# Kernel tuning notes

Hardware: AMD Instinct MI355X
Metric: run time of the kernel (lower is better)

The kernel has to match this reference:

```python
import jax, jax.numpy as jnp
import numpy as np

NUM_USERS = 100000
NUM_ITEMS = 50000
N_NODES = NUM_USERS + NUM_ITEMS
D = 64                 # embed_dim (= user/item/cate embed dims)
NNZ = 2400000          # sparse adjacency nnz (avg degree 16)
B = 4096               # batch size
HIST = 50              # item history length (max)
UHIST = 30             # user history length (max)
MC = 5                 # max categories per item
NC = 1000              # num_cates
CONCAT = 3 * D         # 192 = user/item concat dim
INNER = 2 * CONCAT     # 384 = MLP expansion factor 2
NUM_GNN_LAYERS = 3


def setup_inputs() -> dict:
    ks = jax.random.split(jax.random.key(0), 20)
    emb_table = jax.random.normal(ks[0], (N_NODES, D), jnp.float32) * 0.02
    cate_table = jax.random.normal(ks[1], (NC, D), jnp.float32) * 0.02
    adj_rows = jax.random.randint(ks[2], (NNZ,), 0, N_NODES, jnp.int32)
    adj_cols = jax.random.randint(ks[3], (NNZ,), 0, N_NODES, jnp.int32)
    adj_vals = jax.random.uniform(ks[4], (NNZ,), jnp.float32) * (1.0 / 16.0)
    cates = jax.random.randint(ks[5], (NUM_ITEMS, MC), 0, NC, jnp.int32)
    cate_lens = jax.random.randint(ks[6], (NUM_ITEMS,), 1, MC + 1, jnp.int32)
    users = jax.random.randint(ks[7], (B,), 0, NUM_USERS, jnp.int32)
    items = jax.random.randint(ks[8], (B,), 0, NUM_ITEMS, jnp.int32)
    item_history_matrix = jax.random.randint(ks[9], (B, HIST), 0, NUM_ITEMS, jnp.int32)
    item_history_len = jax.random.randint(ks[10], (B,), 1, HIST + 1, jnp.int32)
    user_history_matrix = jax.random.randint(ks[11], (B, UHIST), 0, NUM_USERS, jnp.int32)
    user_history_len = jax.random.randint(ks[12], (B,), 1, UHIST + 1, jnp.int32)
    # 4 PreNormResidual MLP blocks: [user_mlp, user_mlp_2, item_mlp, item_mlp_2]
    mlp_ln_w = jnp.ones((4, CONCAT), jnp.float32)
    mlp_ln_b = jnp.zeros((4, CONCAT), jnp.float32)
    mlp_w1 = jax.random.normal(ks[13], (4, CONCAT, INNER), jnp.float32) * 0.05
    mlp_b1 = jnp.zeros((4, INNER), jnp.float32)
    mlp_w2 = jax.random.normal(ks[14], (4, INNER, CONCAT), jnp.float32) * 0.05
    mlp_b2 = jnp.zeros((4, CONCAT), jnp.float32)
    return dict(emb_table=emb_table, cate_table=cate_table, adj_vals=adj_vals,
                mlp_ln_w=mlp_ln_w, mlp_ln_b=mlp_ln_b, mlp_w1=mlp_w1, mlp_b1=mlp_b1,
                mlp_w2=mlp_w2, mlp_b2=mlp_b2, adj_rows=adj_rows, adj_cols=adj_cols,
                cates=cates, cate_lens=cate_lens, users=users, items=items,
                item_history_matrix=item_history_matrix, item_history_len=item_history_len,
                user_history_matrix=user_history_matrix, user_history_len=user_history_len)


def _avg_pool(emb, lens):
    # emb: [..., L, D], lens: [...] -> masked mean over L (matches average_pooling)
    L = emb.shape[-2]
    mask = (jnp.arange(L) < lens[..., None]).astype(emb.dtype)[..., None]
    s = jnp.sum(emb * mask, axis=-2)
    c = jnp.sum(mask, axis=-2) + 1e-9
    return s / c


def _layernorm(x, w, b, eps=1e-5):
    mu = jnp.mean(x, axis=-1, keepdims=True)
    var = jnp.mean(jnp.square(x - mu), axis=-1, keepdims=True)
    return (x - mu) * jax.lax.rsqrt(var + eps) * w + b


def _forward(emb_table, cate_table, adj_vals, mlp_ln_w, mlp_ln_b, mlp_w1, mlp_b1,
             mlp_w2, mlp_b2, adj_rows, adj_cols, cates, cate_lens, users, items,
             item_history_matrix, item_history_len, user_history_matrix, user_history_len):
    n = emb_table.shape[0]
    # GNN propagation: mean of [e0, e1, e2, e3], e_{k+1} = A @ e_k (SpMM via segment_sum)
    e = emb_table
    acc = emb_table
    for _ in range(NUM_GNN_LAYERS):
        msgs = adj_vals[:, None] * e[adj_cols]          # [nnz, D]
        e = jax.ops.segment_sum(msgs, adj_rows, num_segments=n)
        acc = acc + e
    gnn = acc / float(NUM_GNN_LAYERS + 1)
    # --- user features ---
    static_u = gnn[users]                               # [B, D]
    hist_item = emb_table[item_history_matrix + NUM_USERS]   # [B, H, D]
    hc = cates[item_history_matrix]                     # [B, H, MC]
    hcl = cate_lens[item_history_matrix]                # [B, H]
    hce = cate_table[hc]                                # [B, H, MC, D]
    avg_cate = _avg_pool(hce, hcl)                      # [B, H, D]
    hist_with_cate = jnp.concatenate([hist_item, avg_cate], axis=-1)  # [B, H, 2D]
    user_hist = _avg_pool(hist_with_cate, item_history_len)           # [B, 2D]
    uf = jnp.concatenate([static_u, user_hist], axis=-1)              # [B, 3D]
    # --- item features ---
    static_i = gnn[items + NUM_USERS]                   # [B, D]
    ice = cate_table[cates[items]]                      # [B, MC, D]
    avg_ic = _avg_pool(ice, cate_lens[items])           # [B, D]
    item_with_cate = jnp.concatenate([static_i, avg_ic], axis=-1)     # [B, 2D]
    hu = emb_table[user_history_matrix]                 # [B, Hu, D]
    item_hist = _avg_pool(hu, user_history_len)         # [B, D]
    itf = jnp.concatenate([item_with_cate, item_hist], axis=-1)       # [B, 3D]
    # --- PreNormResidual MLP blocks ---
    def block(x, i):
        y = _layernorm(x, mlp_ln_w[i], mlp_ln_b[i])
        h = jax.nn.relu(y @ mlp_w1[i] + mlp_b1[i])
        return h @ mlp_w2[i] + mlp_b2[i] + x
    ue = block(uf, 0) + block(uf, 1)
    ie = block(itf, 2) + block(itf, 3)
    ue = ue / jnp.maximum(jnp.linalg.norm(ue, axis=-1, keepdims=True), 1e-12)
    ie = ie / jnp.maximum(jnp.linalg.norm(ie, axis=-1, keepdims=True), 1e-12)
    return ue, ie


def reference(emb_table, cate_table, adj_vals, mlp_ln_w, mlp_ln_b, mlp_w1, mlp_b1,
              mlp_w2, mlp_b2, adj_rows, adj_cols, cates, cate_lens, users, items,
              item_history_matrix, item_history_len, user_history_matrix, user_history_len):
    return _forward(emb_table, cate_table, adj_vals, mlp_ln_w, mlp_ln_b, mlp_w1, mlp_b1,
                    mlp_w2, mlp_b2, adj_rows, adj_cols, cates, cate_lens, users, items,
                    item_history_matrix, item_history_len, user_history_matrix, user_history_len)
```

## Files before the change

### kernel.cpp

```cpp
#include <hip/hip_runtime.h>
#include <hip/hip_bf16.h>
#include <cstdint>
#include <cstddef>

#define NU      100000
#define NN      150000
#define DDIM    64
#define NNZ_C   2400000
#define B_C     4096
#define HIST_C  50
#define UHIST_C 30
#define MC_C    5
#define CDIM    192
#define IDIM    384
#define SCAN_B  147
#define SCAN_N  (SCAN_B * 1024)
#define MAXF    96256
#define CAP     44
#define EDGE_BLKS 1172
#define FEAT_BLKS 2048
#define CONV_BLKS 2304
#define EMBC_BLKS 1172

typedef __bf16 bf16x8 __attribute__((ext_vector_type(8)));
typedef __bf16 bf16x4 __attribute__((ext_vector_type(4)));
typedef float f32x4 __attribute__((ext_vector_type(4)));

__device__ inline float4 ldb(const __bf16* p) {
  bf16x4 v = *(const bf16x4*)p;
  return make_float4((float)v[0], (float)v[1], (float)v[2], (float)v[3]);
}
__device__ inline void stb(__bf16* p, float4 o) {
  bf16x4 v;
  v[0] = (__bf16)o.x; v[1] = (__bf16)o.y; v[2] = (__bf16)o.z; v[3] = (__bf16)o.w;
  *(bf16x4*)p = v;
}

__device__ inline void xr4(float4& a) {
  a.x += __shfl_xor(a.x, 16, 64); a.y += __shfl_xor(a.y, 16, 64);
  a.z += __shfl_xor(a.z, 16, 64); a.w += __shfl_xor(a.w, 16, 64);
  a.x += __shfl_xor(a.x, 32, 64); a.y += __shfl_xor(a.y, 32, 64);
  a.z += __shfl_xor(a.z, 32, 64); a.w += __shfl_xor(a.w, 32, 64);
}

__global__ __launch_bounds__(256) void seedflag_kernel(
    const int* __restrict__ users, const int* __restrict__ items,
    int* __restrict__ sf, int* __restrict__ flag) {
  int t = blockIdx.x * 256 + threadIdx.x;
  if (t >= 2 * B_C) return;
  int s = (t < B_C) ? users[t] : items[t - B_C] + NU;
  sf[s] = 1;
  flag[s] = 1;
}

__global__ __launch_bounds__(256) void mega_kernel(
    const int* __restrict__ rows, const int* __restrict__ cols,
    const float* __restrict__ vals, const int* __restrict__ sf,
    int* __restrict__ flag, int* __restrict__ deg, int2* __restrict__ edgp,
    const float* __restrict__ emb, const float* __restrict__ cate_table,
    const int* __restrict__ cates, const int* __restrict__ cate_lens,
    const int* __restrict__ items, const int* __restrict__ ihm,
    const int* __restrict__ ihl, const int* __restrict__ uhm,
    const int* __restrict__ uhl, float* __restrict__ uf,
    float* __restrict__ itf,
    const float* __restrict__ w1, const float* __restrict__ w2,
    __bf16* __restrict__ w1t, __bf16* __restrict__ w2t,
    __bf16* __restrict__ embbf) {
  int blk = blockIdx.x;
  if (blk < EDGE_BLKS) {
    int base = blk * 2048 + threadIdx.x;
#pragma unroll
    for (int k = 0; k < 8; ++k) {
      int e = base + k * 256;
      if (e < NNZ_C) {
        int r = rows[e];
        int p = atomicAdd(&deg[r], 1);
        if (p < CAP)
          edgp[(size_t)r * CAP + p] = make_int2(cols[e], __float_as_int(vals[e]));
        if (sf[r]) flag[cols[e]] = 1;
      }
    }
  } else if (blk < EDGE_BLKS + FEAT_BLKS) {
    int tid = threadIdx.x;
    int wave = tid >> 6, w = tid & 63, g = w >> 4, li = w & 15;
    int q = (blk - EDGE_BLKS) * 4 + wave;
    if (q < B_C) {
      int b = q;
      int len = ihl[b];
      float4 su = {0.f, 0.f, 0.f, 0.f}, sc = {0.f, 0.f, 0.f, 0.f};
      for (int h = g; h < len; h += 4) {
        int it = ihm[b * HIST_C + h];
        const float4 iv = *(const float4*)(emb + ((size_t)NU + it) * DDIM + li * 4);
        su.x += iv.x; su.y += iv.y; su.z += iv.z; su.w += iv.w;
        int cl = cate_lens[it];
        float4 cs = {0.f, 0.f, 0.f, 0.f};
        for (int c = 0; c < cl; ++c) {
          const float4 cv = *(const float4*)(cate_table + (size_t)cates[it * MC_C + c] * DDIM + li * 4);
          cs.x += cv.x; cs.y += cv.y; cs.z += cv.z; cs.w += cv.w;
        }
        float icl = 1.f / (float)cl;
        sc.x += cs.x * icl; sc.y += cs.y * icl; sc.z += cs.z * icl; sc.w += cs.w * icl;
      }
      xr4(su); xr4(sc);
      float inv = 1.f / (float)len;
      float* urow = uf + (size_t)b * CDIM;
      if (g == 0) {
        float4 o = {su.x * inv, su.y * inv, su.z * inv, su.w * inv};
        *(float4*)(urow + 64 + li * 4) = o;
      } else if (g == 1) {
        float4 o = {sc.x * inv, sc.y * inv, sc.z * inv, sc.w * inv};
        *(float4*)(urow + 128 + li * 4) = o;
      }
    } else {
      int b = q - B_C;
      int it = items[b];
      int cl = cate_lens[it];
      float4 cs = {0.f, 0.f, 0.f, 0.f};
      for (int c = g; c < cl; c += 4) {
        const float4 cv = *(const float4*)(cate_table + (size_t)cates[it * MC_C + c] * DDIM + li * 4);
        cs.x += cv.x; cs.y += cv.y; cs.z += cv.z; cs.w += cv.w;
      }
      int ul = uhl[b];
      float4 hs = {0.f, 0.f, 0.f, 0.f};
      for (int h = g; h < ul; h += 4) {
        const float4 hv = *(const float4*)(emb + (size_t)uhm[b * UHIST_C + h] * DDIM + li * 4);
        hs.x += hv.x; hs.y += hv.y; hs.z += hv.z; hs.w += hv.w;
      }
      xr4(cs); xr4(hs);
      float* irow = itf + (size_t)b * CDIM;
      if (g == 0) {
        float icl = 1.f / (float)cl;
        float4 o = {cs.x * icl, cs.y * icl, cs.z * icl, cs.w * icl};
        *(float4*)(irow + 64 + li * 4) = o;
      } else if (g == 1) {
        float iul = 1.f / (float)ul;
        float4 o = {hs.x * iul, hs.y * iul, hs.z * iul, hs.w * iul};
        *(float4*)(irow + 128 + li * 4) = o;
      }
    }
  } else if (blk < EDGE_BLKS + FEAT_BLKS + CONV_BLKS) {
    int id = (blk - EDGE_BLKS - FEAT_BLKS) * 256 + threadIdx.x;
    if (id < 4 * CDIM * IDIM) {
      int k = id % CDIM;
      int rest = id / CDIM;
      int n = rest % IDIM;
      int p = rest / IDIM;
      w1t[id] = (__bf16)w1[((size_t)(p * CDIM) + k) * IDIM + n];
    } else {
      int id2 = id - 4 * CDIM * IDIM;
      int k = id2 % IDIM;
      int rest = id2 / IDIM;
      int n = rest % CDIM;
      int p = rest / CDIM;
      w2t[id2] = (__bf16)w2[((size_t)(p * IDIM) + k) * CDIM + n];
    }
  } else {
    int base = (blk - EDGE_BLKS - FEAT_BLKS - CONV_BLKS) * 2048 + threadIdx.x;
#pragma unroll
    for (int k = 0; k < 8; ++k) {
      int gidx = base + k * 256;
      if (gidx < 2400000) {
        float4 v = ((const float4*)emb)[gidx];
        stb(embbf + (size_t)gidx * 4, v);
      }
    }
  }
}

__global__ __launch_bounds__(1024) void scan_reduce(
    const int* __restrict__ arr, int* __restrict__ bsums) {
  __shared__ int s[1024];
  int t = threadIdx.x;
  s[t] = arr[blockIdx.x * 1024 + t];
  __syncthreads();
  for (int off = 512; off; off >>= 1) {
    if (t < off) s[t] += s[t + off];
    __syncthreads();
  }
  if (t == 0) bsums[blockIdx.x] = s[0];
}

__global__ __launch_bounds__(1024) void compact_scan(
    int* __restrict__ flag, const int* __restrict__ bsums2,
    int* __restrict__ list, int* __restrict__ cnt) {
  __shared__ int pre[1024];
  __shared__ int s[1024];
  int t = threadIdx.x;
  pre[t] = (t < (int)blockIdx.x) ? bsums2[t] : 0;
  __syncthreads();
  for (int off = 512; off; off >>= 1) {
    if (t < off) pre[t] += pre[t + off];
    __syncthreads();
  }
  int base = pre[0];
  __syncthreads();
  int i = blockIdx.x * 1024 + t;
  int v = flag[i];
  s[t] = v;
  __syncthreads();
  for (int off = 1; off < 1024; off <<= 1) {
    int u = (t >= off) ? s[t - off] : 0;
    __syncthreads();
    s[t] += u;
    __syncthreads();
  }
  int slot = base + s[t] - v;
  if (v) {
    if (slot < MAXF) { list[slot] = i; flag[i] = slot + 1; }
    else flag[i] = 0;
  }
  if (i == SCAN_N - 1) {
    int tot = base + s[t];
    cnt[0] = (tot < MAXF) ? tot : MAXF;
  }
}

__global__ __launch_bounds__(256) void spmm_gather4(
    const __bf16* __restrict__ srcbf, __bf16* __restrict__ dstbf,
    const int* __restrict__ deg, const int2* __restrict__ edgp) {
  int tid = threadIdx.x;
  int wave = tid >> 6, w = tid & 63, g = w >> 4, li = w & 15;
  int r = blockIdx.x * 16 + wave * 4 + g;
  int n = deg[r]; if (n > CAP) n = CAP;
  const int2* ep = edgp + (size_t)r * CAP;
  float4 a0 = {0.f, 0.f, 0.f, 0.f}, a1 = {0.f, 0.f, 0.f, 0.f};
  float4 a2 = {0.f, 0.f, 0.f, 0.f}, a3 = {0.f, 0.f, 0.f, 0.f};
  int j = 0;
  for (; j + 8 <= n; j += 8) {
    int2 e0 = ep[j], e1 = ep[j + 1], e2 = ep[j + 2], e3 = ep[j + 3];
    int2 e4 = ep[j + 4], e5 = ep[j + 5], e6 = ep[j + 6], e7 = ep[j + 7];
    const float4 s0 = ldb(srcbf + (size_t)e0.x * DDIM + li * 4);
    const float4 s1 = ldb(srcbf + (size_t)e1.x * DDIM + li * 4);
    const float4 s2 = ldb(srcbf + (size_t)e2.x * DDIM + li * 4);
    const float4 s3 = ldb(srcbf + (size_t)e3.x * DDIM + li * 4);
    const float4 s4 = ldb(srcbf + (size_t)e4.x * DDIM + li * 4);
    const float4 s5 = ldb(srcbf + (size_t)e5.x * DDIM + li * 4);
    const float4 s6 = ldb(srcbf + (size_t)e6.x * DDIM + li * 4);
    const float4 s7 = ldb(srcbf + (size_t)e7.x * DDIM + li * 4);
    float v0 = __int_as_float(e0.y), v1 = __int_as_float(e1.y);
    float v2 = __int_as_float(e2.y), v3 = __int_as_float(e3.y);
    float v4 = __int_as_float(e4.y), v5 = __int_as_float(e5.y);
    float v6 = __int_as_float(e6.y), v7 = __int_as_float(e7.y);
    a0.x += v0 * s0.x; a0.y += v0 * s0.y; a0.z += v0 * s0.z; a0.w += v0 * s0.w;
    a1.x += v1 * s1.x; a1.y += v1 * s1.y; a1.z += v1 * s1.z; a1.w += v1 * s1.w;
    a2.x += v2 * s2.x; a2.y += v2 * s2.y; a2.z += v2 * s2.z; a2.w += v2 * s2.w;
    a3.x += v3 * s3.x; a3.y += v3 * s3.y; a3.z += v3 * s3.z; a3.w += v3 * s3.w;
    a0.x += v4 * s4.x; a0.y += v4 * s4.y; a0.z += v4 * s4.z; a0.w += v4 * s4.w;
    a1.x += v5 * s5.x; a1.y += v5 * s5.y; a1.z += v5 * s5.z; a1.w += v5 * s5.w;
    a2.x += v6 * s6.x; a2.y += v6 * s6.y; a2.z += v6 * s6.z; a2.w += v6 * s6.w;
    a3.x += v7 * s7.x; a3.y += v7 * s7.y; a3.z += v7 * s7.z; a3.w += v7 * s7.w;
  }
  for (; j + 2 <= n; j += 2) {
    int2 e0 = ep[j], e1 = ep[j + 1];
    const float4 s0 = ldb(srcbf + (size_t)e0.x * DDIM + li * 4);
    const float4 s1 = ldb(srcbf + (size_t)e1.x * DDIM + li * 4);
    float v0 = __int_as_float(e0.y), v1 = __int_as_float(e1.y);
    a0.x += v0 * s0.x; a0.y += v0 * s0.y; a0.z += v0 * s0.z; a0.w += v0 * s0.w;
    a1.x += v1 * s1.x; a1.y += v1 * s1.y; a1.z += v1 * s1.z; a1.w += v1 * s1.w;
  }
  if (j < n) {
    int2 e0 = ep[j];
    const float4 s0 = ldb(srcbf + (size_t)e0.x * DDIM + li * 4);
    float v0 = __int_as_float(e0.y);
    a0.x += v0 * s0.x; a0.y += v0 * s0.y; a0.z += v0 * s0.z; a0.w += v0 * s0.w;
  }
  float4 o = {a0.x + a1.x + a2.x + a3.x, a0.y + a1.y + a2.y + a3.y,
              a0.z + a1.z + a2.z + a3.z, a0.w + a1.w + a2.w + a3.w};
  stb(dstbf + (size_t)r * DDIM + li * 4, o);
}

__global__ __launch_bounds__(256) void spmm_gather4_masked(
    const __bf16* __restrict__ srcbf, __bf16* __restrict__ dstbf,
    const int* __restrict__ deg, const int2* __restrict__ edgp,
    const int* __restrict__ list, const int* __restrict__ cnt) {
  int tid = threadIdx.x;
  int wave = tid >> 6, w = tid & 63, g = w >> 4, li = w & 15;
  int p = blockIdx.x * 16 + wave * 4 + g;
  if (p >= cnt[0]) return;
  int r = list[p];
  int n = deg[r]; if (n > CAP) n = CAP;
  const int2* ep = edgp + (size_t)r * CAP;
  float4 a0 = {0.f, 0.f, 0.f, 0.f}, a1 = {0.f, 0.f, 0.f, 0.f};
  float4 a2 = {0.f, 0.f, 0.f, 0.f}, a3 = {0.f, 0.f, 0.f, 0.f};
  int j = 0;
  for (; j + 8 <= n; j += 8) {
    int2 e0 = ep[j], e1 = ep[j + 1], e2 = ep[j + 2], e3 = ep[j + 3];
    int2 e4 = ep[j + 4], e5 = ep[j + 5], e6 = ep[j + 6], e7 = ep[j + 7];
    const float4 s0 = ldb(srcbf + (size_t)e0.x * DDIM + li * 4);
    const float4 s1 = ldb(srcbf + (size_t)e1.x * DDIM + li * 4);
    const float4 s2 = ldb(srcbf + (size_t)e2.x * DDIM + li * 4);
    const float4 s3 = ldb(srcbf + (size_t)e3.x * DDIM + li * 4);
    const float4 s4 = ldb(srcbf + (size_t)e4.x * DDIM + li * 4);
    const float4 s5 = ldb(srcbf + (size_t)e5.x * DDIM + li * 4);
    const float4 s6 = ldb(srcbf + (size_t)e6.x * DDIM + li * 4);
    const float4 s7 = ldb(srcbf + (size_t)e7.x * DDIM + li * 4);
    float v0 = __int_as_float(e0.y), v1 = __int_as_float(e1.y);
    float v2 = __int_as_float(e2.y), v3 = __int_as_float(e3.y);
    float v4 = __int_as_float(e4.y), v5 = __int_as_float(e5.y);
    float v6 = __int_as_float(e6.y), v7 = __int_as_float(e7.y);
    a0.x += v0 * s0.x; a0.y += v0 * s0.y; a0.z += v0 * s0.z; a0.w += v0 * s0.w;
    a1.x += v1 * s1.x; a1.y += v1 * s1.y; a1.z += v1 * s1.z; a1.w += v1 * s1.w;
    a2.x += v2 * s2.x; a2.y += v2 * s2.y; a2.z += v2 * s2.z; a2.w += v2 * s2.w;
    a3.x += v3 * s3.x; a3.y += v3 * s3.y; a3.z += v3 * s3.z; a3.w += v3 * s3.w;
    a0.x += v4 * s4.x; a0.y += v4 * s4.y; a0.z += v4 * s4.z; a0.w += v4 * s4.w;
    a1.x += v5 * s5.x; a1.y += v5 * s5.y; a1.z += v5 * s5.z; a1.w += v5 * s5.w;
    a2.x += v6 * s6.x; a2.y += v6 * s6.y; a2.z += v6 * s6.z; a2.w += v6 * s6.w;
    a3.x += v7 * s7.x; a3.y += v7 * s7.y; a3.z += v7 * s7.z; a3.w += v7 * s7.w;
  }
  for (; j + 2 <= n; j += 2) {
    int2 e0 = ep[j], e1 = ep[j + 1];
    const float4 s0 = ldb(srcbf + (size_t)e0.x * DDIM + li * 4);
    const float4 s1 = ldb(srcbf + (size_t)e1.x * DDIM + li * 4);
    float v0 = __int_as_float(e0.y), v1 = __int_as_float(e1.y);
    a0.x += v0 * s0.x; a0.y += v0 * s0.y; a0.z += v0 * s0.z; a0.w += v0 * s0.w;
    a1.x += v1 * s1.x; a1.y += v1 * s1.y; a1.z += v1 * s1.z; a1.w += v1 * s1.w;
  }
  if (j < n) {
    int2 e0 = ep[j];
    const float4 s0 = ldb(srcbf + (size_t)e0.x * DDIM + li * 4);
    float v0 = __int_as_float(e0.y);
    a0.x += v0 * s0.x; a0.y += v0 * s0.y; a0.z += v0 * s0.z; a0.w += v0 * s0.w;
  }
  float4 o = {a0.x + a1.x + a2.x + a3.x, a0.y + a1.y + a2.y + a3.y,
              a0.z + a1.z + a2.z + a3.z, a0.w + a1.w + a2.w + a3.w};
  stb(dstbf + (size_t)p * DDIM + li * 4, o);
}

__global__ __launch_bounds__(256) void seed_finish(
    const float* __restrict__ emb, const __bf16* __restrict__ e1bf,
    const __bf16* __restrict__ e2cbf, const int* __restrict__ flag,
    const int* __restrict__ deg, const int2* __restrict__ edgp,
    const int* __restrict__ users, const int* __restrict__ items,
    float* __restrict__ uf, float* __restrict__ itf) {
  int tid = threadIdx.x;
  int wave = tid >> 6, w = tid & 63, g = w >> 4, li = w & 15;
  int qi = blockIdx.x * 16 + wave * 4 + g;
  int s = (qi < B_C) ? users[qi] : items[qi - B_C] + NU;
  int n = deg[s]; if (n > CAP) n = CAP;
  const int2* ep = edgp + (size_t)s * CAP;
  float4 a0 = {0.f, 0.f, 0.f, 0.f}, a1 = {0.f, 0.f, 0.f, 0.f};
  float4 a2 = {0.f, 0.f, 0.f, 0.f}, a3 = {0.f, 0.f, 0.f, 0.f};
  int j = 0;
  for (; j + 4 <= n; j += 4) {
    int2 e0 = ep[j], e1v = ep[j + 1], e2v = ep[j + 2], e3v = ep[j + 3];
    int p0 = flag[e0.x] - 1;  p0 = p0 > 0 ? p0 : 0;
    int p1 = flag[e1v.x] - 1; p1 = p1 > 0 ? p1 : 0;
    int p2 = flag[e2v.x] - 1; p2 = p2 > 0 ? p2 : 0;
    int p3 = flag[e3v.x] - 1; p3 = p3 > 0 ? p3 : 0;
    const float4 s0 = ldb(e2cbf + (size_t)p0 * DDIM + li * 4);
    const float4 s1 = ldb(e2cbf + (size_t)p1 * DDIM + li * 4);
    const float4 s2 = ldb(e2cbf + (size_t)p2 * DDIM + li * 4);
    const float4 s3 = ldb(e2cbf + (size_t)p3 * DDIM + li * 4);
    float v0 = __int_as_float(e0.y), v1 = __int_as_float(e1v.y);
    float v2 = __int_as_float(e2v.y), v3 = __int_as_float(e3v.y);
    a0.x += v0 * s0.x; a0.y += v0 * s0.y; a0.z += v0 * s0.z; a0.w += v0 * s0.w;
    a1.x += v1 * s1.x; a1.y += v1 * s1.y; a1.z += v1 * s1.z; a1.w += v1 * s1.w;
    a2.x += v2 * s2.x; a2.y += v2 * s2.y; a2.z += v2 * s2.z; a2.w += v2 * s2.w;
    a3.x += v3 * s3.x; a3.y += v3 * s3.y; a3.z += v3 * s3.z; a3.w += v3 * s3.w;
  }
  for (; j < n; ++j) {
    int2 e0 = ep[j];
    int p0 = flag[e0.x] - 1; p0 = p0 > 0 ? p0 : 0;
    const float4 s0 = ldb(e2cbf + (size_t)p0 * DDIM + li * 4);
    float v0 = __int_as_float(e0.y);
    a0.x += v0 * s0.x; a0.y += v0 * s0.y; a0.z += v0 * s0.z; a0.w += v0 * s0.w;
  }
  const float4 e0v = *(const float4*)(emb + (size_t)s * DDIM + li * 4);
  const float4 e1r = ldb(e1bf + (size_t)s * DDIM + li * 4);
  int ps = flag[s] - 1; ps = ps > 0 ? ps : 0;
  const float4 e2v = ldb(e2cbf + (size_t)ps * DDIM + li * 4);
  float4 o;
  o.x = (e0v.x + e1r.x + e2v.x + a0.x + a1.x + a2.x + a3.x) * 0.25f;
  o.y = (e0v.y + e1r.y + e2v.y + a0.y + a1.y + a2.y + a3.y) * 0.25f;
  o.z = (e0v.z + e1r.z + e2v.z + a0.z + a1.z + a2.z + a3.z) * 0.25f;
  o.w = (e0v.w + e1r.w + e2v.w + a0.w + a1.w + a2.w + a3.w) * 0.25f;
  float* row = (qi < B_C) ? uf + (size_t)qi * CDIM : itf + (size_t)(qi - B_C) * CDIM;
  *(float4*)(row + li * 4) = o;
}

__global__ __launch_bounds__(64) void ln_kernel(
    const float* __restrict__ uf, const float* __restrict__ itf,
    const float* __restrict__ lnw, const float* __restrict__ lnb,
    __bf16* __restrict__ ybf) {
  int b = blockIdx.x, p = blockIdx.y, t = threadIdx.x;
  const float* x = ((p < 2) ? uf : itf) + (size_t)b * CDIM;
  float v0 = x[t], v1 = x[t + 64], v2 = x[t + 128];
  float s = v0 + v1 + v2;
#pragma unroll
  for (int off = 32; off; off >>= 1) s += __shfl_down(s, off, 64);
  float mu = __shfl(s, 0, 64) * (1.f / 192.f);
  float d0 = v0 - mu, d1 = v1 - mu, d2 = v2 - mu;
  float q = d0 * d0 + d1 * d1 + d2 * d2;
#pragma unroll
  for (int off = 32; off; off >>= 1) q += __shfl_down(q, off, 64);
  float var = __shfl(q, 0, 64) * (1.f / 192.f);
  float rs = 1.f / sqrtf(var + 1e-5f);
  __bf16* yo = ybf + ((size_t)p * B_C + b) * CDIM;
  const float* w = lnw + p * CDIM;
  const float* bb = lnb + p * CDIM;
  yo[t]       = (__bf16)(d0 * rs * w[t]       + bb[t]);
  yo[t + 64]  = (__bf16)(d1 * rs * w[t + 64]  + bb[t + 64]);
  yo[t + 128] = (__bf16)(d2 * rs * w[t + 128] + bb[t + 128]);
}

__global__ __launch_bounds__(256) void gemm1_mfma(
    const __bf16* __restrict__ ybf, const __bf16* __restrict__ w1t,
    const float* __restrict__ b1, __bf16* __restrict__ hbf) {
  int p = blockIdx.z;
  const __bf16* A = ybf + (size_t)p * B_C * CDIM;
  const __bf16* Bt = w1t + (size_t)p * IDIM * CDIM;
  int wave = threadIdx.x >> 6, lane = threadIdx.x & 63;
  int q = lane >> 4, n16 = lane & 15;
  int r0 = blockIdx.x * 64 + wave * 16;
  int c0 = blockIdx.y * 64;
  f32x4 acc[4] = {{0.f, 0.f, 0.f, 0.f}, {0.f, 0.f, 0.f, 0.f},
                  {0.f, 0.f, 0.f, 0.f}, {0.f, 0.f, 0.f, 0.f}};
#pragma unroll
  for (int k0 = 0; k0 < CDIM; k0 += 32) {
    bf16x8 a = *(const bf16x8*)(A + (size_t)(r0 + n16) * CDIM + k0 + q * 8);
#pragma unroll
    for (int c = 0; c < 4; ++c) {
      bf16x8 b = *(const bf16x8*)(Bt + (size_t)(c0 + c * 16 + n16) * CDIM + k0 + q * 8);
      acc[c] = __builtin_amdgcn_mfma_f32_16x16x32_bf16(a, b, acc[c], 0, 0, 0);
    }
  }
#pragma unroll
  for (int c = 0; c < 4; ++c) {
    int col = c0 + c * 16 + n16;
    float bias = b1[p * IDIM + col];
#pragma unroll
    for (int r = 0; r < 4; ++r) {
      int row = r0 + q * 4 + r;
      float v = fmaxf(acc[c][r] + bias, 0.f);
      hbf[((size_t)p * B_C + row) * IDIM + col] = (__bf16)v;
    }
  }
}

__global__ __launch_bounds__(256) void gemm2_mfma(
    const __bf16* __restrict__ hbf, const __bf16* __restrict__ w2t,
    const float* __restrict__ b2, const float* __restrict__ uf,
    const float* __restrict__ itf, float* __restrict__ zu, float* __restrict__ zi) {
  int s = blockIdx.z;
  const float* X = s ? itf : uf;
  float* Z = s ? zi : zu;
  int wave = threadIdx.x >> 6, lane = threadIdx.x & 63;
  int q = lane >> 4, n16 = lane & 15;
  int r0 = blockIdx.x * 64 + wave * 16;
  int c0 = blockIdx.y * 64;
  f32x4 acc[4] = {{0.f, 0.f, 0.f, 0.f}, {0.f, 0.f, 0.f, 0.f},
                  {0.f, 0.f, 0.f, 0.f}, {0.f, 0.f, 0.f, 0.f}};
#pragma unroll
  for (int pi = 0; pi < 2; ++pi) {
    int p = s * 2 + pi;
    const __bf16* A = hbf + (size_t)p * B_C * IDIM;
    const __bf16* Bt = w2t + (size_t)p * CDIM * IDIM;
#pragma unroll
    for (int k0 = 0; k0 < IDIM; k0 += 32) {
      bf16x8 a = *(const bf16x8*)(A + (size_t)(r0 + n16) * IDIM + k0 + q * 8);
#pragma unroll
      for (int c = 0; c < 4; ++c) {
        bf16x8 b = *(const bf16x8*)(Bt + (size_t)(c0 + c * 16 + n16) * IDIM + k0 + q * 8);
        acc[c] = __builtin_amdgcn_mfma_f32_16x16x32_bf16(a, b, acc[c], 0, 0, 0);
      }
    }
  }
#pragma unroll
  for (int c = 0; c < 4; ++c) {
    int col = c0 + c * 16 + n16;
    float bs = b2[(s * 2) * CDIM + col] + b2[(s * 2 + 1) * CDIM + col];
#pragma unroll
    for (int r = 0; r < 4; ++r) {
      int row = r0 + q * 4 + r;
      float xv = X[(size_t)row * CDIM + col];
      Z[(size_t)row * CDIM + col] = acc[c][r] + bs + 2.f * xv;
    }
  }
}

__global__ __launch_bounds__(64) void norm_kernel(
    const float* __restrict__ zu, const float* __restrict__ zi,
    float* __restrict__ out) {
  int b = blockIdx.x, s = blockIdx.y, t = threadIdx.x;
  const float* z = (s ? zi : zu) + (size_t)b * CDIM;
  float v0 = z[t], v1 = z[t + 64], v2 = z[t + 128];
  float q = v0 * v0 + v1 * v1 + v2 * v2;
#pragma unroll
  for (int off = 32; off; off >>= 1) q += __shfl_down(q, off, 64);
  float n = sqrtf(__shfl(q, 0, 64));
  float inv = 1.f / fmaxf(n, 1e-12f);
  float* o = out + (size_t)s * B_C * CDIM + (size_t)b * CDIM;
  o[t] = v0 * inv;
  o[t + 64] = v1 * inv;
  o[t + 128] = v2 * inv;
}

extern "C" void kernel_launch(void* const* d_in, const int* in_sizes, int n_in,
                              void* d_out, int out_size, void* d_ws, size_t ws_size,
                              hipStream_t stream) {
  const float* emb   = (const float*)d_in[0];
  const float* cate  = (const float*)d_in[1];
  const float* avals = (const float*)d_in[2];
  const float* lnw   = (const float*)d_in[3];
  const float* lnb   = (const float*)d_in[4];
  const float* w1    = (const float*)d_in[5];
  const float* b1    = (const float*)d_in[6];
  const float* w2    = (const float*)d_in[7];
  const float* b2    = (const float*)d_in[8];
  const int* arows   = (const int*)d_in[9];
  const int* acols   = (const int*)d_in[10];
  const int* cates_  = (const int*)d_in[11];
  const int* clens   = (const int*)d_in[12];
  const int* users   = (const int*)d_in[13];
  const int* items   = (const int*)d_in[14];
  const int* ihm     = (const int*)d_in[15];
  const int* ihl     = (const int*)d_in[16];
  const int* uhm     = (const int*)d_in[17];
  const int* uhl     = (const int*)d_in[18];
  float* out = (float*)d_out;

  float* W = (float*)d_ws;
  __bf16* e1bf   = (__bf16*)W;
  __bf16* embbf  = (__bf16*)(W + 4816896);
  __bf16* e2cbf  = (__bf16*)(W + 4816896);
  int2*   edgp   = (int2*)(W + 9616896);
  int*    deg    = (int*)(W + 22863360);
  int*    flag   = (int*)(W + 23013888);
  int*    sf     = (int*)(W + 23164416);
  int*    cnt    = (int*)(W + 23314944);
  int*    list   = (int*)(W + 23315008);
  int*    bsums2 = (int*)(W + 23411264);
  float*  uf     = W + 23411520;
  float*  itf    = W + 24197952;
  __bf16* w1t    = (__bf16*)(W + 24984384);
  __bf16* w2t    = (__bf16*)(W + 25131840);
  __bf16* ybf = (__bf16*)(W + 9616896);
  __bf16* hbf = (__bf16*)(W + 9616896 + 1572864);
  float* zu = W + 4816896;
  float* zi = W + 4816896 + 786432;

  (void)hipMemsetAsync(deg, 0, (3 * 150528 + 64) * sizeof(int), stream);

  seedflag_kernel<<<(2 * B_C + 255) / 256, 256, 0, stream>>>(users, items, sf, flag);

  mega_kernel<<<EDGE_BLKS + FEAT_BLKS + CONV_BLKS + EMBC_BLKS, 256, 0, stream>>>(
      arows, acols, avals, sf, flag, deg, edgp,
      emb, cate, cates_, clens, items, ihm, ihl, uhm, uhl, uf, itf,
      w1, w2, w1t, w2t, embbf);

  scan_reduce<<<SCAN_B, 1024, 0, stream>>>(flag, bsums2);
  compact_scan<<<SCAN_B, 1024, 0, stream>>>(flag, bsums2, list, cnt);

  spmm_gather4<<<NN / 16, 256, 0, stream>>>(embbf, e1bf, deg, edgp);
  spmm_gather4_masked<<<MAXF / 16, 256, 0, stream>>>(e1bf, e2cbf, deg, edgp, list, cnt);
  seed_finish<<<(2 * B_C) / 16, 256, 0, stream>>>(emb, e1bf, e2cbf, flag, deg,
                                                  edgp, users, items, uf, itf);

  ln_kernel<<<dim3(B_C, 4), 64, 0, stream>>>(uf, itf, lnw, lnb, ybf);
  gemm1_mfma<<<dim3(B_C / 64, IDIM / 64, 4), 256, 0, stream>>>(ybf, w1t, b1, hbf);
  gemm2_mfma<<<dim3(B_C / 64, CDIM / 64, 2), 256, 0, stream>>>(hbf, w2t, b2, uf, itf, zu, zi);
  norm_kernel<<<dim3(B_C, 2), 64, 0, stream>>>(zu, zi, out);
}
```

Baseline: 474.6 us.

## Drop frontier compaction scans and fuse L2 normalization into second GEMM

Removes the two-kernel prefix-scan compaction of flagged nodes. The second-layer SpMM now runs over all nodes in a dense grid and skips unflagged rows by zeroing their degree, which lets seed_finish index e2 directly by node id instead of going through flag indirection. The second MLP GEMM now computes all 192 output columns per block and applies the row L2 normalization in its epilogue, eliminating the separate norm kernel and the z round-trip through memory. This trades two launches and scan work for a larger dense grid of mostly-empty rows, and for fewer GEMM blocks that each hold more accumulator registers.

Result: slower. 501.9 us (+5.7%).

```diff
diff --git a/kernel.cpp b/kernel.cpp
--- a/kernel.cpp
+++ b/kernel.cpp
@@ -13,9 +13,7 @@
 #define MC_C    5
 #define CDIM    192
 #define IDIM    384
-#define SCAN_B  147
-#define SCAN_N  (SCAN_B * 1024)
-#define MAXF    96256
+#define NNP     150528
 #define CAP     44
 #define EDGE_BLKS 1172
 #define FEAT_BLKS 2048
@@ -164,54 +162,6 @@
         stb(embbf + (size_t)gidx * 4, v);
       }
     }
-  }
-}
-
-__global__ __launch_bounds__(1024) void scan_reduce(
-    const int* __restrict__ arr, int* __restrict__ bsums) {
-  __shared__ int s[1024];
-  int t = threadIdx.x;
-  s[t] = arr[blockIdx.x * 1024 + t];
-  __syncthreads();
-  for (int off = 512; off; off >>= 1) {
-    if (t < off) s[t] += s[t + off];
-    __syncthreads();
-  }
-  if (t == 0) bsums[blockIdx.x] = s[0];
-}
-
-__global__ __launch_bounds__(1024) void compact_scan(
-    int* __restrict__ flag, const int* __restrict__ bsums2,
-    int* __restrict__ list, int* __restrict__ cnt) {
-  __shared__ int pre[1024];
-  __shared__ int s[1024];
-  int t = threadIdx.x;
-  pre[t] = (t < (int)blockIdx.x) ? bsums2[t] : 0;
-  __syncthreads();
-  for (int off = 512; off; off >>= 1) {
-    if (t < off) pre[t] += pre[t + off];
-    __syncthreads();
-  }
-  int base = pre[0];
-  __syncthreads();
-  int i = blockIdx.x * 1024 + t;
-  int v = flag[i];
-  s[t] = v;
-  __syncthreads();
-  for (int off = 1; off < 1024; off <<= 1) {
-    int u = (t >= off) ? s[t - off] : 0;
-    __syncthreads();
-    s[t] += u;
-    __syncthreads();
-  }
-  int slot = base + s[t] - v;
-  if (v) {
-    if (slot < MAXF) { list[slot] = i; flag[i] = slot + 1; }
-    else flag[i] = 0;
-  }
-  if (i == SCAN_N - 1) {
-    int tot = base + s[t];
-    cnt[0] = (tot < MAXF) ? tot : MAXF;
   }
 }
 
@@ -269,16 +219,15 @@
   stb(dstbf + (size_t)r * DDIM + li * 4, o);
 }
 
-__global__ __launch_bounds__(256) void spmm_gather4_masked(
-    const __bf16* __restrict__ srcbf, __bf16* __restrict__ dstbf,
+__global__ __launch_bounds__(256) void spmm_e2_flag(
+    const __bf16* __restrict__ srcbf, __bf16* __restrict__ e2bf,
     const int* __restrict__ deg, const int2* __restrict__ edgp,
-    const int* __restrict__ list, const int* __restrict__ cnt) {
+    const int* __restrict__ flag) {
   int tid = threadIdx.x;
   int wave = tid >> 6, w = tid & 63, g = w >> 4, li = w & 15;
-  int p = blockIdx.x * 16 + wave * 4 + g;
-  if (p >= cnt[0]) return;
-  int r = list[p];
-  int n = deg[r]; if (n > CAP) n = CAP;
+  int r = blockIdx.x * 16 + wave * 4 + g;
+  int n = flag[r] ? deg[r] : 0;
+  if (n > CAP) n = CAP;
   const int2* ep = edgp + (size_t)r * CAP;
   float4 a0 = {0.f, 0.f, 0.f, 0.f}, a1 = {0.f, 0.f, 0.f, 0.f};
   float4 a2 = {0.f, 0.f, 0.f, 0.f}, a3 = {0.f, 0.f, 0.f, 0.f};
@@ -323,15 +272,15 @@
   }
   float4 o = {a0.x + a1.x + a2.x + a3.x, a0.y + a1.y + a2.y + a3.y,
               a0.z + a1.z + a2.z + a3.z, a0.w + a1.w + a2.w + a3.w};
-  stb(dstbf + (size_t)p * DDIM + li * 4, o);
+  stb(e2bf + (size_t)r * DDIM + li * 4, o);
 }
 
 __global__ __launch_bounds__(256) void seed_finish(
     const float* __restrict__ emb, const __bf16* __restrict__ e1bf,
-    const __bf16* __restrict__ e2cbf, const int* __restrict__ flag,
-    const int* __restrict__ deg, const int2* __restrict__ edgp,
-    const int* __restrict__ users, const int* __restrict__ items,
-    float* __restrict__ uf, float* __restrict__ itf) {
+    const __bf16* __restrict__ e2bf, const int* __restrict__ deg,
+    const int2* __restrict__ edgp, const int* __restrict__ users,
+    const int* __restrict__ items, float* __restrict__ uf,
+    float* __restrict__ itf) {
   int tid = threadIdx.x;
   int wave = tid >> 6, w = tid & 63, g = w >> 4, li = w & 15;
   int qi = blockIdx.x * 16 + wave * 4 + g;
@@ -343,14 +292,10 @@
   int j = 0;
   for (; j + 4 <= n; j += 4) {
     int2 e0 = ep[j], e1v = ep[j + 1], e2v = ep[j + 2], e3v = ep[j + 3];
-    int p0 = flag[e0.x] - 1;  p0 = p0 > 0 ? p0 : 0;
-    int p1 = flag[e1v.x] - 1; p1 = p1 > 0 ? p1 : 0;
-    int p2 = flag[e2v.x] - 1; p2 = p2 > 0 ? p2 : 0;
-    int p3 = flag[e3v.x] - 1; p3 = p3 > 0 ? p3 : 0;
-    const float4 s0 = ldb(e2cbf + (size_t)p0 * DDIM + li * 4);
-    const float4 s1 = ldb(e2cbf + (size_t)p1 * DDIM + li * 4);
-    const float4 s2 = ldb(e2cbf + (size_t)p2 * DDIM + li * 4);
-    const float4 s3 = ldb(e2cbf + (size_t)p3 * DDIM + li * 4);
+    const float4 s0 = ldb(e2bf + (size_t)e0.x * DDIM + li * 4);
+    const float4 s1 = ldb(e2bf + (size_t)e1v.x * DDIM + li * 4);
+    const float4 s2 = ldb(e2bf + (size_t)e2v.x * DDIM + li * 4);
+    const float4 s3 = ldb(e2bf + (size_t)e3v.x * DDIM + li * 4);
     float v0 = __int_as_float(e0.y), v1 = __int_as_float(e1v.y);
     float v2 = __int_as_float(e2v.y), v3 = __int_as_float(e3v.y);
     a0.x += v0 * s0.x; a0.y += v0 * s0.y; a0.z += v0 * s0.z; a0.w += v0 * s0.w;
@@ -360,15 +305,13 @@
   }
   for (; j < n; ++j) {
     int2 e0 = ep[j];
-    int p0 = flag[e0.x] - 1; p0 = p0 > 0 ? p0 : 0;
-    const float4 s0 = ldb(e2cbf + (size_t)p0 * DDIM + li * 4);
+    const float4 s0 = ldb(e2bf + (size_t)e0.x * DDIM + li * 4);
     float v0 = __int_as_float(e0.y);
     a0.x += v0 * s0.x; a0.y += v0 * s0.y; a0.z += v0 * s0.z; a0.w += v0 * s0.w;
   }
   const float4 e0v = *(const float4*)(emb + (size_t)s * DDIM + li * 4);
   const float4 e1r = ldb(e1bf + (size_t)s * DDIM + li * 4);
-  int ps = flag[s] - 1; ps = ps > 0 ? ps : 0;
-  const float4 e2v = ldb(e2cbf + (size_t)ps * DDIM + li * 4);
+  const float4 e2v = ldb(e2bf + (size_t)s * DDIM + li * 4);
   float4 o;
   o.x = (e0v.x + e1r.x + e2v.x + a0.x + a1.x + a2.x + a3.x) * 0.25f;
   o.y = (e0v.y + e1r.y + e2v.y + a0.y + a1.y + a2.y + a3.y) * 0.25f;
@@ -437,19 +380,18 @@
   }
 }
 
-__global__ __launch_bounds__(256) void gemm2_mfma(
+__global__ __launch_bounds__(256) void gemm2norm_mfma(
     const __bf16* __restrict__ hbf, const __bf16* __restrict__ w2t,
     const float* __restrict__ b2, const float* __restrict__ uf,
-    const float* __restrict__ itf, float* __restrict__ zu, float* __restrict__ zi) {
-  int s = blockIdx.z;
+    const float* __restrict__ itf, float* __restrict__ out) {
+  int s = blockIdx.y;
   const float* X = s ? itf : uf;
-  float* Z = s ? zi : zu;
   int wave = threadIdx.x >> 6, lane = threadIdx.x & 63;
   int q = lane >> 4, n16 = lane & 15;
   int r0 = blockIdx.x * 64 + wave * 16;
-  int c0 = blockIdx.y * 64;
-  f32x4 acc[4] = {{0.f, 0.f, 0.f, 0.f}, {0.f, 0.f, 0.f, 0.f},
-                  {0.f, 0.f, 0.f, 0.f}, {0.f, 0.f, 0.f, 0.f}};
+  f32x4 acc[12];
+#pragma unroll
+  for (int c = 0; c < 12; ++c) acc[c] = (f32x4){0.f, 0.f, 0.f, 0.f};
 #pragma unroll
   for (int pi = 0; pi < 2; ++pi) {
     int p = s * 2 + pi;
@@ -459,40 +401,49 @@
     for (int k0 = 0; k0 < IDIM; k0 += 32) {
       bf16x8 a = *(const bf16x8*)(A + (size_t)(r0 + n16) * IDIM + k0 + q * 8);
 #pragma unroll
-      for (int c = 0; c < 4; ++c) {
-        bf16x8 b = *(const bf16x8*)(Bt + (size_t)(c0 + c * 16 + n16) * IDIM + k0 + q * 8);
+      for (int c = 0; c < 12; ++c) {
+        bf16x8 b = *(const bf16x8*)(Bt + (size_t)(c * 16 + n16) * IDIM + k0 + q * 8);
         acc[c] = __builtin_amdgcn_mfma_f32_16x16x32_bf16(a, b, acc[c], 0, 0, 0);
       }
     }
   }
-#pragma unroll
-  for (int c = 0; c < 4; ++c) {
-    int col = c0 + c * 16 + n16;
+  float ss0 = 0.f, ss1 = 0.f, ss2 = 0.f, ss3 = 0.f;
+#pragma unroll
+  for (int c = 0; c < 12; ++c) {
+    int col = c * 16 + n16;
     float bs = b2[(s * 2) * CDIM + col] + b2[(s * 2 + 1) * CDIM + col];
 #pragma unroll
     for (int r = 0; r < 4; ++r) {
       int row = r0 + q * 4 + r;
-      float xv = X[(size_t)row * CDIM + col];
-      Z[(size_t)row * CDIM + col] = acc[c][r] + bs + 2.f * xv;
-    }
-  }
-}
-
-__global__ __launch_bounds__(64) void norm_kernel(
-    const float* __restrict__ zu, const float* __restrict__ zi,
-    float* __restrict__ out) {
-  int b = blockIdx.x, s = blockIdx.y, t = threadIdx.x;
-  const float* z = (s ? zi : zu) + (size_t)b * CDIM;
-  float v0 = z[t], v1 = z[t + 64], v2 = z[t + 128];
-  float q = v0 * v0 + v1 * v1 + v2 * v2;
-#pragma unroll
-  for (int off = 32; off; off >>= 1) q += __shfl_down(q, off, 64);
-  float n = sqrtf(__shfl(q, 0, 64));
-  float inv = 1.f / fmaxf(n, 1e-12f);
-  float* o = out + (size_t)s * B_C * CDIM + (size_t)b * CDIM;
-  o[t] = v0 * inv;
-  o[t + 64] = v1 * inv;
-  o[t + 128] = v2 * inv;
+      float z = acc[c][r] + bs + 2.f * X[(size_t)row * CDIM + col];
+      acc[c][r] = z;
+      if (r == 0) ss0 += z * z;
+      else if (r == 1) ss1 += z * z;
+      else if (r == 2) ss2 += z * z;
+      else ss3 += z * z;
+    }
+  }
+#pragma unroll
+  for (int off = 1; off < 16; off <<= 1) {
+    ss0 += __shfl_xor(ss0, off, 64);
+    ss1 += __shfl_xor(ss1, off, 64);
+    ss2 += __shfl_xor(ss2, off, 64);
+    ss3 += __shfl_xor(ss3, off, 64);
+  }
+  float inv0 = 1.f / fmaxf(sqrtf(ss0), 1e-12f);
+  float inv1 = 1.f / fmaxf(sqrtf(ss1), 1e-12f);
+  float inv2 = 1.f / fmaxf(sqrtf(ss2), 1e-12f);
+  float inv3 = 1.f / fmaxf(sqrtf(ss3), 1e-12f);
+  float* o = out + (size_t)s * B_C * CDIM;
+#pragma unroll
+  for (int c = 0; c < 12; ++c) {
+    int col = c * 16 + n16;
+    int row = r0 + q * 4;
+    o[(size_t)(row + 0) * CDIM + col] = acc[c][0] * inv0;
+    o[(size_t)(row + 1) * CDIM + col] = acc[c][1] * inv1;
+    o[(size_t)(row + 2) * CDIM + col] = acc[c][2] * inv2;
+    o[(size_t)(row + 3) * CDIM + col] = acc[c][3] * inv3;
+  }
 }
 
 extern "C" void kernel_launch(void* const* d_in, const int* in_sizes, int n_in,
@@ -522,24 +473,19 @@
   float* W = (float*)d_ws;
   __bf16* e1bf   = (__bf16*)W;
   __bf16* embbf  = (__bf16*)(W + 4816896);
-  __bf16* e2cbf  = (__bf16*)(W + 4816896);
-  int2*   edgp   = (int2*)(W + 9616896);
-  int*    deg    = (int*)(W + 22863360);
-  int*    flag   = (int*)(W + 23013888);
-  int*    sf     = (int*)(W + 23164416);
-  int*    cnt    = (int*)(W + 23314944);
-  int*    list   = (int*)(W + 23315008);
-  int*    bsums2 = (int*)(W + 23411264);
-  float*  uf     = W + 23411520;
-  float*  itf    = W + 24197952;
-  __bf16* w1t    = (__bf16*)(W + 24984384);
-  __bf16* w2t    = (__bf16*)(W + 25131840);
-  __bf16* ybf = (__bf16*)(W + 9616896);
-  __bf16* hbf = (__bf16*)(W + 9616896 + 1572864);
-  float* zu = W + 4816896;
-  float* zi = W + 4816896 + 786432;
-
-  (void)hipMemsetAsync(deg, 0, (3 * 150528 + 64) * sizeof(int), stream);
+  __bf16* e2bf   = (__bf16*)(W + 4816896);
+  int2*   edgp   = (int2*)(W + 9633792);
+  int*    deg    = (int*)(W + 22880256);
+  int*    flag   = (int*)(W + 23030784);
+  int*    sf     = (int*)(W + 23181312);
+  float*  uf     = W + 23331840;
+  float*  itf    = W + 24118272;
+  __bf16* w1t    = (__bf16*)(W + 24904704);
+  __bf16* w2t    = (__bf16*)(W + 25052160);
+  __bf16* ybf = (__bf16*)(W + 9633792);
+  __bf16* hbf = (__bf16*)(W + 9633792 + 1572864);
+
+  (void)hipMemsetAsync(deg, 0, (3 * NNP) * sizeof(int), stream);
 
   seedflag_kernel<<<(2 * B_C + 255) / 256, 256, 0, stream>>>(users, items, sf, flag);
 
@@ -548,16 +494,12 @@
       emb, cate, cates_, clens, items, ihm, ihl, uhm, uhl, uf, itf,
       w1, w2, w1t, w2t, embbf);
 
-  scan_reduce<<<SCAN_B, 1024, 0, stream>>>(flag, bsums2);
-  compact_scan<<<SCAN_B, 1024, 0, stream>>>(flag, bsums2, list, cnt);
-
   spmm_gather4<<<NN / 16, 256, 0, stream>>>(embbf, e1bf, deg, edgp);
-  spmm_gather4_masked<<<MAXF / 16, 256, 0, stream>>>(e1bf, e2cbf, deg, edgp, list, cnt);
-  seed_finish<<<(2 * B_C) / 16, 256, 0, stream>>>(emb, e1bf, e2cbf, flag, deg,
-                                                  edgp, users, items, uf, itf);
+  spmm_e2_flag<<<NN / 16, 256, 0, stream>>>(e1bf, e2bf, deg, edgp, flag);
+  seed_finish<<<(2 * B_C) / 16, 256, 0, stream>>>(emb, e1bf, e2bf, deg, edgp,
+                                                  users, items, uf, itf);
 
   ln_kernel<<<dim3(B_C, 4), 64, 0, stream>>>(uf, itf, lnw, lnb, ybf);
   gemm1_mfma<<<dim3(B_C / 64, IDIM / 64, 4), 256, 0, stream>>>(ybf, w1t, b1, hbf);
-  gemm2_mfma<<<dim3(B_C / 64, CDIM / 64, 2), 256, 0, stream>>>(hbf, w2t, b2, uf, itf, zu, zi);
-  norm_kernel<<<dim3(B_C, 2), 64, 0, stream>>>(zu, zi, out);
-}
+  gemm2norm_mfma<<<dim3(B_C / 64, 2), 256, 0, stream>>>(hbf, w2t, b2, uf, itf, out);
+}
```
